# Optimization experiments

Measured on AMD Instinct MI355X. Metric: run time of the kernel, lower is better.

Reference implementation:

```python
import jax, jax.numpy as jnp
import numpy as np

B, N, L, D_IN, D = 32, 2048, 32768, 4, 64


def setup_inputs() -> dict:
    key = jax.random.key(0)
    ks = jax.random.split(key, 10)
    s = 0.05  # modest init scale for params
    return {
        "pred_node": jax.random.normal(ks[0], (B, N, D_IN), jnp.float32),
        "line_param": jax.random.normal(ks[1], (B, L, 4), jnp.float32),
        "W_embed": jax.random.normal(ks[2], (D_IN, D), jnp.float32) * s,
        "b_embed": jnp.zeros((D,), jnp.float32),
        "W1": jax.random.normal(ks[3], (2 * D, D), jnp.float32) * s,
        "b1": jnp.zeros((D,), jnp.float32),
        "W2": jax.random.normal(ks[4], (D, 4), jnp.float32) * s,
        "b2": jnp.zeros((4,), jnp.float32),
        "edge_src": jax.random.randint(ks[5], (B, L), 0, N, jnp.int32),
        "edge_dst": jax.random.randint(ks[6], (B, L), 0, N, jnp.int32),
    }


def reference(pred_node, line_param, W_embed, b_embed, W1, b1, W2, b2,
              edge_src, edge_dst):
    # node_feat_to_line_feat: Linear(4 -> d_model) over all nodes at once
    node_feat = jnp.einsum("bni,id->bnd", pred_node, W_embed) + b_embed  # (B,N,D)

    # Batched gather of node-feature pairs per edge (replaces Python loops)
    fi = jnp.take_along_axis(node_feat, edge_src[..., None].astype(jnp.int32), axis=1)  # (B,L,D)
    fj = jnp.take_along_axis(node_feat, edge_dst[..., None].astype(jnp.int32), axis=1)  # (B,L,D)
    combined = jnp.concatenate([fi, fj], axis=-1)  # (B,L,2D)

    # line_pred_head: Linear(2D->D) -> ReLU -> Dropout(eval: identity) -> Linear(D->4)
    h = jax.nn.relu(jnp.einsum("ble,ed->bld", combined, W1) + b1)
    line_pred = jnp.einsum("bld,do->blo", h, W2) + b2  # (B,L,4)

    # Cols 0,1 copied from line_param; cols 2,3 from the prediction head
    out = jnp.concatenate([line_param[..., :2], line_pred[..., 2:4]], axis=-1)
    return out
```

## Files before the change

### kernel.cpp

```cpp
#include <hip/hip_runtime.h>
#include <stdint.h>

#define B_ 32
#define N_ 2048
#define L_ 32768


static __device__ __forceinline__ float4 f4fma(float s, float4 a, float4 b) {
    return make_float4(fmaf(s, a.x, b.x), fmaf(s, a.y, b.y),
                       fmaf(s, a.z, b.z), fmaf(s, a.w, b.w));
}

__global__ void prep_kernel(const float* __restrict__ W_embed,
                            const float* __restrict__ b_embed,
                            const float* __restrict__ W1,
                            const float* __restrict__ b1,
                            const float* __restrict__ W2,
                            float* __restrict__ wc) {
    int d = threadIdx.x;
    float acc1[4] = {0.f, 0.f, 0.f, 0.f};
    float acc2[4] = {0.f, 0.f, 0.f, 0.f};
    float bb = 0.f;
    for (int k = 0; k < 64; ++k) {
        float w1a = W1[k * 64 + d];
        float w1b = W1[(64 + k) * 64 + d];
        float be = b_embed[k];
        bb = fmaf(be, w1a + w1b, bb);
#pragma unroll
        for (int i = 0; i < 4; ++i) {
            float we = W_embed[i * 64 + k];
            acc1[i] = fmaf(we, w1a, acc1[i]);
            acc2[i] = fmaf(we, w1b, acc2[i]);
        }
    }
#pragma unroll
    for (int i = 0; i < 4; ++i) {
        wc[i * 64 + d] = acc1[i];
        wc[256 + i * 64 + d] = acc2[i];
    }
    wc[512 + d] = bb + b1[d];
    wc[640 + 2 * d] = W2[d * 4 + 2];
    wc[641 + 2 * d] = W2[d * 4 + 3];
}

__global__ __launch_bounds__(256, 3) void edge_kernel(
    const float4* __restrict__ pred_node,
    const float* __restrict__ wc,
    const int* __restrict__ esrc, const int* __restrict__ edst,
    const float2* __restrict__ lp2,
    const float* __restrict__ b2,
    float4* __restrict__ out) {
    __shared__ float4 spn[N_];

    int tid = threadIdx.x;
    int k = tid & 7;
    int g = tid >> 3;

    int bid = blockIdx.x;
    int x = bid & 7;
    int i = bid >> 3;
    int b = x + 8 * (i >> 6);
    int j = i & 63;

    const float4* pnb = pred_node + b * N_;
#pragma unroll
    for (int q = 0; q < 8; ++q) {
        int idx = tid + q * 256;
        spn[idx] = pnb[idx];
    }

    const float4* wcv = (const float4*)wc;
    float4 c1a[4], c1b[4], c2a[4], c2b[4];
#pragma unroll
    for (int r = 0; r < 4; ++r) {
        c1a[r] = wcv[r * 16 + k * 2];
        c1b[r] = wcv[r * 16 + k * 2 + 1];
        c2a[r] = wcv[64 + r * 16 + k * 2];
        c2b[r] = wcv[64 + r * 16 + k * 2 + 1];
    }
    float4 bc0 = wcv[128 + k * 2];
    float4 bc1 = wcv[128 + k * 2 + 1];
    float4 w20 = wcv[160 + k * 4];
    float4 w21 = wcv[160 + k * 4 + 1];
    float4 w22 = wcv[160 + k * 4 + 2];
    float4 w23 = wcv[160 + k * 4 + 3];
    float bias2 = b2[2], bias3 = b2[3];

    int ebase = b * L_ + j * 512 + g;

    int sarr[16], tarr[16];
#pragma unroll
    for (int p = 0; p < 16; ++p) {
        int e = ebase + p * 32;
        sarr[p] = esrc[e];
        tarr[p] = edst[e];
    }

    __syncthreads();

#pragma unroll
    for (int p = 0; p < 16; ++p) {
        int e = ebase + p * 32;
        float4 ps = spn[sarr[p]];
        float4 pt = spn[tarr[p]];

        float4 h0 = bc0, h1 = bc1;
        h0 = f4fma(ps.x, c1a[0], h0); h1 = f4fma(ps.x, c1b[0], h1);
        h0 = f4fma(ps.y, c1a[1], h0); h1 = f4fma(ps.y, c1b[1], h1);
        h0 = f4fma(ps.z, c1a[2], h0); h1 = f4fma(ps.z, c1b[2], h1);
        h0 = f4fma(ps.w, c1a[3], h0); h1 = f4fma(ps.w, c1b[3], h1);
        h0 = f4fma(pt.x, c2a[0], h0); h1 = f4fma(pt.x, c2b[0], h1);
        h0 = f4fma(pt.y, c2a[1], h0); h1 = f4fma(pt.y, c2b[1], h1);
        h0 = f4fma(pt.z, c2a[2], h0); h1 = f4fma(pt.z, c2b[2], h1);
        h0 = f4fma(pt.w, c2a[3], h0); h1 = f4fma(pt.w, c2b[3], h1);
        h0.x = fmaxf(h0.x, 0.f); h0.y = fmaxf(h0.y, 0.f);
        h0.z = fmaxf(h0.z, 0.f); h0.w = fmaxf(h0.w, 0.f);
        h1.x = fmaxf(h1.x, 0.f); h1.y = fmaxf(h1.y, 0.f);
        h1.z = fmaxf(h1.z, 0.f); h1.w = fmaxf(h1.w, 0.f);

        float acc2, acc3;
        acc2 = h0.x * w20.x;              acc3 = h0.x * w20.y;
        acc2 = fmaf(h0.y, w20.z, acc2);   acc3 = fmaf(h0.y, w20.w, acc3);
        acc2 = fmaf(h0.z, w21.x, acc2);   acc3 = fmaf(h0.z, w21.y, acc3);
        acc2 = fmaf(h0.w, w21.z, acc2);   acc3 = fmaf(h0.w, w21.w, acc3);
        acc2 = fmaf(h1.x, w22.x, acc2);   acc3 = fmaf(h1.x, w22.y, acc3);
        acc2 = fmaf(h1.y, w22.z, acc2);   acc3 = fmaf(h1.y, w22.w, acc3);
        acc2 = fmaf(h1.z, w23.x, acc2);   acc3 = fmaf(h1.z, w23.y, acc3);
        acc2 = fmaf(h1.w, w23.z, acc2);   acc3 = fmaf(h1.w, w23.w, acc3);

        acc2 += __shfl_xor(acc2, 1); acc3 += __shfl_xor(acc3, 1);
        acc2 += __shfl_xor(acc2, 2); acc3 += __shfl_xor(acc3, 2);
        acc2 += __shfl_xor(acc2, 4); acc3 += __shfl_xor(acc3, 4);

        if (k == 0) {
            float2 v = lp2[(size_t)e * 2];
            out[e] = make_float4(v.x, v.y, acc2 + bias2, acc3 + bias3);
        }
    }
}

extern "C" void kernel_launch(void* const* d_in, const int* in_sizes, int n_in,
                              void* d_out, int out_size, void* d_ws, size_t ws_size,
                              hipStream_t stream) {
    const float* pred_node = (const float*)d_in[0];
    const float* line_param = (const float*)d_in[1];
    const float* W_embed = (const float*)d_in[2];
    const float* b_embed = (const float*)d_in[3];
    const float* W1 = (const float*)d_in[4];
    const float* b1 = (const float*)d_in[5];
    const float* W2 = (const float*)d_in[6];
    const float* b2 = (const float*)d_in[7];
    const int* esrc = (const int*)d_in[8];
    const int* edst = (const int*)d_in[9];
    float* out = (float*)d_out;

    float* wc = (float*)d_ws;

    prep_kernel<<<1, 64, 0, stream>>>(W_embed, b_embed, W1, b1, W2, wc);
    edge_kernel<<<2048, 256, 0, stream>>>((const float4*)pred_node, wc,
                                          esrc, edst,
                                          (const float2*)line_param, b2,
                                          (float4*)out);
}
```

Before: 128.7 us.

## Give each thread whole edges and stream folded weights instead of splitting features

The work split changes from 8 threads per edge, each holding 8 hidden features with a shuffle reduction, to one thread per edge looping over all 64 hidden units for 4 edges at once. The prep kernel now packs the folded weights per hidden unit (12 floats) so each iteration reads them as uniform float4 loads. The grid is halved to 1024 blocks so each block covers 1024 edges, and launch bounds target 4 blocks per CU. This removes the shuffles and the idle lanes at output, and writes coalesced float4 outputs from every lane. In exchange each block does 4x more arithmetic per edge-thread and issues scalar weight loads every iteration, with fewer blocks to hide the shared-memory fill.

```diff
diff --git a/kernel.cpp b/kernel.cpp
--- a/kernel.cpp
+++ b/kernel.cpp
@@ -5,11 +5,6 @@
 #define N_ 2048
 #define L_ 32768
 
-
-static __device__ __forceinline__ float4 f4fma(float s, float4 a, float4 b) {
-    return make_float4(fmaf(s, a.x, b.x), fmaf(s, a.y, b.y),
-                       fmaf(s, a.z, b.z), fmaf(s, a.w, b.w));
-}
 
 __global__ void prep_kernel(const float* __restrict__ W_embed,
                             const float* __restrict__ b_embed,
@@ -33,17 +28,19 @@
             acc2[i] = fmaf(we, w1b, acc2[i]);
         }
     }
+    float* w = wc + d * 12;
 #pragma unroll
     for (int i = 0; i < 4; ++i) {
-        wc[i * 64 + d] = acc1[i];
-        wc[256 + i * 64 + d] = acc2[i];
+        w[i] = acc1[i];
+        w[4 + i] = acc2[i];
     }
-    wc[512 + d] = bb + b1[d];
-    wc[640 + 2 * d] = W2[d * 4 + 2];
-    wc[641 + 2 * d] = W2[d * 4 + 3];
+    w[8] = bb + b1[d];
+    w[9] = W2[d * 4 + 2];
+    w[10] = W2[d * 4 + 3];
+    w[11] = 0.f;
 }
 
-__global__ __launch_bounds__(256, 3) void edge_kernel(
+__global__ __launch_bounds__(256, 4) void edge_kernel(
     const float4* __restrict__ pred_node,
     const float* __restrict__ wc,
     const int* __restrict__ esrc, const int* __restrict__ edst,
@@ -53,14 +50,11 @@
     __shared__ float4 spn[N_];
 
     int tid = threadIdx.x;
-    int k = tid & 7;
-    int g = tid >> 3;
-
     int bid = blockIdx.x;
     int x = bid & 7;
     int i = bid >> 3;
-    int b = x + 8 * (i >> 6);
-    int j = i & 63;
+    int b = x + 8 * (i >> 5);
+    int j = i & 31;
 
     const float4* pnb = pred_node + b * N_;
 #pragma unroll
@@ -69,73 +63,60 @@
         spn[idx] = pnb[idx];
     }
 
-    const float4* wcv = (const float4*)wc;
-    float4 c1a[4], c1b[4], c2a[4], c2b[4];
+    int ebase = b * L_ + j * 1024 + tid;
+
+    int sa[4], ta[4];
 #pragma unroll
-    for (int r = 0; r < 4; ++r) {
-        c1a[r] = wcv[r * 16 + k * 2];
-        c1b[r] = wcv[r * 16 + k * 2 + 1];
-        c2a[r] = wcv[64 + r * 16 + k * 2];
-        c2b[r] = wcv[64 + r * 16 + k * 2 + 1];
+    for (int p = 0; p < 4; ++p) {
+        sa[p] = esrc[ebase + p * 256];
+        ta[p] = edst[ebase + p * 256];
     }
-    float4 bc0 = wcv[128 + k * 2];
-    float4 bc1 = wcv[128 + k * 2 + 1];
-    float4 w20 = wcv[160 + k * 4];
-    float4 w21 = wcv[160 + k * 4 + 1];
-    float4 w22 = wcv[160 + k * 4 + 2];
-    float4 w23 = wcv[160 + k * 4 + 3];
     float bias2 = b2[2], bias3 = b2[3];
-
-    int ebase = b * L_ + j * 512 + g;
-
-    int sarr[16], tarr[16];
-#pragma unroll
-    for (int p = 0; p < 16; ++p) {
-        int e = ebase + p * 32;
-        sarr[p] = esrc[e];
-        tarr[p] = edst[e];
-    }
 
     __syncthreads();
 
+    float4 ps[4], pt[4];
 #pragma unroll
-    for (int p = 0; p < 16; ++p) {
-        int e = ebase + p * 32;
-        float4 ps = spn[sarr[p]];
-        float4 pt = spn[tarr[p]];
+    for (int p = 0; p < 4; ++p) {
+        ps[p] = spn[sa[p]];
+        pt[p] = spn[ta[p]];
+    }
 
-        float4 h0 = bc0, h1 = bc1;
-        h0 = f4fma(ps.x, c1a[0], h0); h1 = f4fma(ps.x, c1b[0], h1);
-        h0 = f4fma(ps.y, c1a[1], h0); h1 = f4fma(ps.y, c1b[1], h1);
-        h0 = f4fma(ps.z, c1a[2], h0); h1 = f4fma(ps.z, c1b[2], h1);
-        h0 = f4fma(ps.w, c1a[3], h0); h1 = f4fma(ps.w, c1b[3], h1);
-        h0 = f4fma(pt.x, c2a[0], h0); h1 = f4fma(pt.x, c2b[0], h1);
-        h0 = f4fma(pt.y, c2a[1], h0); h1 = f4fma(pt.y, c2b[1], h1);
-        h0 = f4fma(pt.z, c2a[2], h0); h1 = f4fma(pt.z, c2b[2], h1);
-        h0 = f4fma(pt.w, c2a[3], h0); h1 = f4fma(pt.w, c2b[3], h1);
-        h0.x = fmaxf(h0.x, 0.f); h0.y = fmaxf(h0.y, 0.f);
-        h0.z = fmaxf(h0.z, 0.f); h0.w = fmaxf(h0.w, 0.f);
-        h1.x = fmaxf(h1.x, 0.f); h1.y = fmaxf(h1.y, 0.f);
-        h1.z = fmaxf(h1.z, 0.f); h1.w = fmaxf(h1.w, 0.f);
+    float a2[4] = {bias2, bias2, bias2, bias2};
+    float a3[4] = {bias3, bias3, bias3, bias3};
 
-        float acc2, acc3;
-        acc2 = h0.x * w20.x;              acc3 = h0.x * w20.y;
-        acc2 = fmaf(h0.y, w20.z, acc2);   acc3 = fmaf(h0.y, w20.w, acc3);
-        acc2 = fmaf(h0.z, w21.x, acc2);   acc3 = fmaf(h0.z, w21.y, acc3);
-        acc2 = fmaf(h0.w, w21.z, acc2);   acc3 = fmaf(h0.w, w21.w, acc3);
-        acc2 = fmaf(h1.x, w22.x, acc2);   acc3 = fmaf(h1.x, w22.y, acc3);
-        acc2 = fmaf(h1.y, w22.z, acc2);   acc3 = fmaf(h1.y, w22.w, acc3);
-        acc2 = fmaf(h1.z, w23.x, acc2);   acc3 = fmaf(h1.z, w23.y, acc3);
-        acc2 = fmaf(h1.w, w23.z, acc2);   acc3 = fmaf(h1.w, w23.w, acc3);
+    const float4* wq = (const float4*)wc;
+#pragma unroll 1
+    for (int fc = 0; fc < 16; ++fc) {
+#pragma unroll
+        for (int f = 0; f < 4; ++f) {
+            int fi = fc * 4 + f;
+            float4 wa = wq[fi * 3 + 0];
+            float4 wb = wq[fi * 3 + 1];
+            float4 wx = wq[fi * 3 + 2];
+#pragma unroll
+            for (int p = 0; p < 4; ++p) {
+                float h = wx.x;
+                h = fmaf(ps[p].x, wa.x, h);
+                h = fmaf(ps[p].y, wa.y, h);
+                h = fmaf(ps[p].z, wa.z, h);
+                h = fmaf(ps[p].w, wa.w, h);
+                h = fmaf(pt[p].x, wb.x, h);
+                h = fmaf(pt[p].y, wb.y, h);
+                h = fmaf(pt[p].z, wb.z, h);
+                h = fmaf(pt[p].w, wb.w, h);
+                h = fmaxf(h, 0.f);
+                a2[p] = fmaf(h, wx.y, a2[p]);
+                a3[p] = fmaf(h, wx.z, a3[p]);
+            }
+        }
+    }
 
-        acc2 += __shfl_xor(acc2, 1); acc3 += __shfl_xor(acc3, 1);
-        acc2 += __shfl_xor(acc2, 2); acc3 += __shfl_xor(acc3, 2);
-        acc2 += __shfl_xor(acc2, 4); acc3 += __shfl_xor(acc3, 4);
-
-        if (k == 0) {
-            float2 v = lp2[(size_t)e * 2];
-            out[e] = make_float4(v.x, v.y, acc2 + bias2, acc3 + bias3);
-        }
+#pragma unroll
+    for (int p = 0; p < 4; ++p) {
+        int e = ebase + p * 256;
+        float2 v = lp2[(size_t)e * 2];
+        out[e] = make_float4(v.x, v.y, a2[p], a3[p]);
     }
 }
 
@@ -157,7 +138,7 @@
     float* wc = (float*)d_ws;
 
     prep_kernel<<<1, 64, 0, stream>>>(W_embed, b_embed, W1, b1, W2, wc);
-    edge_kernel<<<2048, 256, 0, stream>>>((const float4*)pred_node, wc,
+    edge_kernel<<<1024, 256, 0, stream>>>((const float4*)pred_node, wc,
                                           esrc, edst,
                                           (const float2*)line_param, b2,
                                           (float4*)out);
```

After: 115.5 us. -10.3%, faster.
